# Performance work log

Measured on AMD Instinct MI355X. Metric: run time of the kernel, lower is better.

The kernel has to match this reference:

```python
import jax, jax.numpy as jnp
import numpy as np

N_ENT = 100000


def setup_inputs() -> dict:
    key = jax.random.key(0)
    ks = jax.random.split(key, 10)
    B, D, O, R, E = 50000, 128, 128, 8, 200000
    return {
        "embeddings": jax.random.normal(ks[0], (N_ENT, D), dtype=jnp.float32),
        "head_e": jax.random.normal(ks[1], (B, D), dtype=jnp.float32),
        "tail_e": jax.random.normal(ks[2], (B, D), dtype=jnp.float32),
        "relation_kernel": jax.random.normal(ks[3], (R, D, O), dtype=jnp.float32),
        "self_kernel": jax.random.normal(ks[4], (D, O), dtype=jnp.float32),
        "edge_val": jax.random.uniform(ks[5], (R, E), dtype=jnp.float32),
        "head_idx": jax.random.randint(ks[6], (B,), 0, N_ENT, dtype=jnp.int32),
        "tail_idx": jax.random.randint(ks[7], (B,), 0, N_ENT, dtype=jnp.int32),
        "edge_src": jax.random.randint(ks[8], (R, E), 0, N_ENT, dtype=jnp.int32),
        "edge_dst": jax.random.randint(ks[9], (R, E), 0, N_ENT, dtype=jnp.int32),
    }


def reference(embeddings, head_e, tail_e, relation_kernel, self_kernel,
              edge_val, head_idx, tail_idx, edge_src, edge_dst):
    # Per-relation SpMM: sum_emb[r, row] = sum_{edges e of r with src=row} val[e] * embeddings[dst[e]]
    def spmm(src, dst, val):
        return jax.ops.segment_sum(embeddings[dst] * val[:, None], src,
                                   num_segments=embeddings.shape[0])
    sum_emb = jax.vmap(spmm)(edge_src, edge_dst, edge_val)  # [R, N, D]

    head_update = jnp.take(sum_emb, head_idx, axis=1)  # [R, B, D]
    tail_update = jnp.take(sum_emb, tail_idx, axis=1)  # [R, B, D]

    head_output = head_e @ self_kernel + jnp.einsum('rbd,rdo->bo', head_update, relation_kernel)
    tail_output = tail_e @ self_kernel + jnp.einsum('rbd,rdo->bo', tail_update, relation_kernel)
    return (jax.nn.sigmoid(head_output), jax.nn.sigmoid(tail_output))
```

## Files before the change

### kernel.cpp

```cpp
#include <hip/hip_runtime.h>
#include <hip/hip_bf16.h>
#include <math.h>

#define N_ENT 100000
#define NB    50000
#define NE    200000
#define RR    8
#define NETOT (RR * NE)
#define NSEG  (RR * N_ENT)

typedef float f32x4  __attribute__((ext_vector_type(4)));
typedef short s16x8  __attribute__((ext_vector_type(8)));

__device__ __forceinline__ void split2(float x, short& h, short& l)
{
    unsigned uh = __float_as_uint(x) & 0xffff0000u;
    h = (short)(uh >> 16);
    float r = x - __uint_as_float(uh);
    l = (short)(__float_as_uint(r) >> 16);
}

__global__ __launch_bounds__(256)
void ktconv_k(const float* __restrict__ rel_k, const float* __restrict__ self_k,
              short* __restrict__ Kth, short* __restrict__ Ktl)
{
    const int r = blockIdx.x;
    const float* src = (r < 8) ? rel_k + (size_t)r * 16384 : self_k;
    short* oh = Kth + (size_t)r * 16384;
    short* ol = Ktl + (size_t)r * 16384;
    for (int i = 0; i < 64; ++i) {
        int ix = i * 256 + threadIdx.x;
        int d = ix >> 7, o = ix & 127;
        short h, l;
        split2(src[ix], h, l);
        oh[o * 128 + d] = h;
        ol[o * 128 + d] = l;
    }
}

template<bool FINAL, bool ACCUM>
__global__ __launch_bounds__(256)
void gemm_mfma_k(const float* __restrict__ X, int xstride,
                 const short* __restrict__ Kth, const short* __restrict__ Ktl,
                 int nkc,
                 const float* __restrict__ Abuf, const int* __restrict__ idx,
                 float* __restrict__ out, int nrows)
{
    __shared__ short Bh[128][136];
    __shared__ short Bl[128][136];

    const int t     = threadIdx.x;
    const int wv    = t >> 6;
    const int lane  = t & 63;
    const int col16 = lane & 15;
    const int g     = lane >> 4;
    const int rowbase = blockIdx.x * 128 + wv * 32;

    f32x4 acc[2][8];
#pragma unroll
    for (int m = 0; m < 2; ++m)
#pragma unroll
        for (int c = 0; c < 8; ++c) acc[m][c] = (f32x4){0.f, 0.f, 0.f, 0.f};

    for (int kc = 0; kc < nkc; ++kc) {
        __syncthreads();
        {
            const s16x8* gh = (const s16x8*)(Kth + (size_t)kc * 16384);
            const s16x8* gl = (const s16x8*)(Ktl + (size_t)kc * 16384);
#pragma unroll
            for (int i = 0; i < 8; ++i) {
                int f = t + i * 256;
                int o = f >> 4, c = f & 15;
                *(s16x8*)&Bh[o][c * 8] = gh[f];
                *(s16x8*)&Bl[o][c * 8] = gl[f];
            }
        }
        __syncthreads();

#pragma unroll
        for (int s = 0; s < 4; ++s) {
            s16x8 ah[2], al[2];
#pragma unroll
            for (int m = 0; m < 2; ++m) {
                int r = rowbase + m * 16 + col16;
                if (r > nrows - 1) r = nrows - 1;
                const float* xp = X + (size_t)r * xstride + kc * 128 + s * 32 + g * 8;
                float4 u0 = *(const float4*)xp;
                float4 u1 = *(const float4*)(xp + 4);
                float u[8] = {u0.x, u0.y, u0.z, u0.w, u1.x, u1.y, u1.z, u1.w};
#pragma unroll
                for (int j = 0; j < 8; ++j) {
                    short h, l; split2(u[j], h, l);
                    ah[m][j] = h; al[m][j] = l;
                }
            }
#pragma unroll
            for (int c = 0; c < 8; ++c) {
                s16x8 bh = *(const s16x8*)&Bh[c * 16 + col16][s * 32 + g * 8];
                s16x8 bl = *(const s16x8*)&Bl[c * 16 + col16][s * 32 + g * 8];
#pragma unroll
                for (int m = 0; m < 2; ++m) {
                    acc[m][c] = __builtin_amdgcn_mfma_f32_16x16x32_bf16(ah[m], bh, acc[m][c], 0, 0, 0);
                    acc[m][c] = __builtin_amdgcn_mfma_f32_16x16x32_bf16(ah[m], bl, acc[m][c], 0, 0, 0);
                    acc[m][c] = __builtin_amdgcn_mfma_f32_16x16x32_bf16(al[m], bh, acc[m][c], 0, 0, 0);
                }
            }
        }
    }

#pragma unroll
    for (int m = 0; m < 2; ++m) {
#pragma unroll
        for (int j = 0; j < 4; ++j) {
            int row = rowbase + m * 16 + g * 4 + j;
            if (row >= nrows) continue;
            float* op = out + (size_t)row * 128;
            if (FINAL) {
                int gi = idx[row];
                const float* Ar = Abuf + (size_t)gi * 128;
#pragma unroll
                for (int c = 0; c < 8; ++c) {
                    int col = c * 16 + col16;
                    float x = acc[m][c][j] + Ar[col];
                    op[col] = 1.f / (1.f + __expf(-x));
                }
            } else if (ACCUM) {
#pragma unroll
                for (int c = 0; c < 8; ++c) {
                    int col = c * 16 + col16;
                    op[col] += acc[m][c][j];
                }
            } else {
#pragma unroll
                for (int c = 0; c < 8; ++c)
                    op[c * 16 + col16] = acc[m][c][j];
            }
        }
    }
}

__global__ __launch_bounds__(256)
void count_k(const int* __restrict__ edge_src, unsigned* __restrict__ cnt)
{
    int g = blockIdx.x * 256 + threadIdx.x;
    int r = g / NE;
    int src = edge_src[g];
    atomicAdd(&cnt[r * N_ENT + src], 1u);
}

__global__ __launch_bounds__(256)
void scan1_k(const unsigned* __restrict__ cnt, unsigned* __restrict__ offs,
             unsigned* __restrict__ bsum)
{
    __shared__ unsigned s[256];
    const int t = threadIdx.x;
    const int base = blockIdx.x * 1024;
    unsigned v[4], sum = 0;
#pragma unroll
    for (int i = 0; i < 4; ++i) {
        int ix = base + t * 4 + i;
        v[i] = (ix < NSEG) ? cnt[ix] : 0u;
        sum += v[i];
    }
    s[t] = sum; __syncthreads();
    for (int off = 1; off < 256; off <<= 1) {
        unsigned x = (t >= off) ? s[t - off] : 0u;
        __syncthreads();
        s[t] += x;
        __syncthreads();
    }
    unsigned run = s[t] - sum;
#pragma unroll
    for (int i = 0; i < 4; ++i) {
        int ix = base + t * 4 + i;
        if (ix < NSEG) offs[ix] = run;
        run += v[i];
    }
    if (t == 255) bsum[blockIdx.x] = s[255];
}

__global__ __launch_bounds__(256)
void scan2_k(unsigned* __restrict__ bsum, int nb)
{
    __shared__ unsigned s[256];
    __shared__ unsigned carry;
    const int t = threadIdx.x;
    if (t == 0) carry = 0;
    __syncthreads();
    for (int base = 0; base < nb; base += 256) {
        unsigned v = (base + t < nb) ? bsum[base + t] : 0u;
        s[t] = v; __syncthreads();
        for (int off = 1; off < 256; off <<= 1) {
            unsigned x = (t >= off) ? s[t - off] : 0u;
            __syncthreads();
            s[t] += x;
            __syncthreads();
        }
        unsigned tot = s[255];
        unsigned excl = s[t] - v + carry;
        if (base + t < nb) bsum[base + t] = excl;
        __syncthreads();
        if (t == 0) carry += tot;
        __syncthreads();
    }
}

__global__ __launch_bounds__(256)
void scan3_k(unsigned* __restrict__ offs, const unsigned* __restrict__ bsum)
{
    const int base = blockIdx.x * 1024;
    unsigned add = bsum[blockIdx.x];
#pragma unroll
    for (int i = 0; i < 4; ++i) {
        int ix = base + threadIdx.x * 4 + i;
        if (ix < NSEG) offs[ix] += add;
    }
    if (blockIdx.x == 0 && threadIdx.x == 0) offs[NSEG] = NETOT;
}

__global__ __launch_bounds__(256)
void fill_k(const int* __restrict__ edge_src, const int* __restrict__ edge_dst,
            const float* __restrict__ edge_val,
            const unsigned* __restrict__ offs, unsigned* __restrict__ cursor,
            int2* __restrict__ recs)
{
    int g = blockIdx.x * 256 + threadIdx.x;
    int r = g / NE;
    int src = edge_src[g];
    int seg = r * N_ENT + src;
    unsigned pos = offs[seg] + atomicAdd(&cursor[seg], 1u);
    int2 rec;
    rec.x = edge_dst[g];
    rec.y = __float_as_int(edge_val[g]);
    recs[pos] = rec;
}

template<int NR>
__global__ __launch_bounds__(256)
void segsum_k(const unsigned* __restrict__ offs_r, const int2* __restrict__ recs,
              const float* __restrict__ emb, float* __restrict__ B)
{
    constexpr int T = 4;
    const int s    = (blockIdx.x * 256 + threadIdx.x) >> 6;
    const int lane = threadIdx.x & 63;
    if (s >= N_ENT) return;

    unsigned e0[NR]; int n[NR];
#pragma unroll
    for (int j = 0; j < NR; ++j) {
        unsigned a = offs_r[(size_t)j * N_ENT + s];
        unsigned b = offs_r[(size_t)j * N_ENT + s + 1];
        e0[j] = a; n[j] = (int)(b - a);
    }

    int2 rec[NR][T];
#pragma unroll
    for (int j = 0; j < NR; ++j)
#pragma unroll
        for (int i = 0; i < T; ++i)
            if (i < n[j]) rec[j][i] = recs[e0[j] + i];

    float2 y[NR][T];
#pragma unroll
    for (int j = 0; j < NR; ++j)
#pragma unroll
        for (int i = 0; i < T; ++i)
            if (i < n[j])
                y[j][i] = *(const float2*)(emb + (size_t)rec[j][i].x * 128 + lane * 2);

    float2 acc[NR];
#pragma unroll
    for (int j = 0; j < NR; ++j) acc[j] = (float2){0.f, 0.f};
#pragma unroll
    for (int j = 0; j < NR; ++j)
#pragma unroll
        for (int i = 0; i < T; ++i)
            if (i < n[j]) {
                float v = __int_as_float(rec[j][i].y);
                acc[j].x = fmaf(v, y[j][i].x, acc[j].x);
                acc[j].y = fmaf(v, y[j][i].y, acc[j].y);
            }

#pragma unroll
    for (int j = 0; j < NR; ++j) {
        for (int i = T; i < n[j]; ++i) {
            int2 rc = recs[e0[j] + i];
            float v = __int_as_float(rc.y);
            float2 yy = *(const float2*)(emb + (size_t)rc.x * 128 + lane * 2);
            acc[j].x = fmaf(v, yy.x, acc[j].x);
            acc[j].y = fmaf(v, yy.y, acc[j].y);
        }
    }

#pragma unroll
    for (int j = 0; j < NR; ++j)
        *(float2*)(B + ((size_t)s * NR + j) * 128 + lane * 2) = acc[j];
}

static void launch_segsum(int nr, const unsigned* offs_r, const int2* recs,
                          const float* emb, float* B, hipStream_t stream)
{
    dim3 blk(256);
    const int blocks = (N_ENT * 64) / 256;
    switch (nr) {
    case 1: segsum_k<1><<<blocks, blk, 0, stream>>>(offs_r, recs, emb, B); break;
    case 2: segsum_k<2><<<blocks, blk, 0, stream>>>(offs_r, recs, emb, B); break;
    case 3: segsum_k<3><<<blocks, blk, 0, stream>>>(offs_r, recs, emb, B); break;
    default: segsum_k<4><<<blocks, blk, 0, stream>>>(offs_r, recs, emb, B); break;
    }
}

extern "C" void kernel_launch(void* const* d_in, const int* in_sizes, int n_in,
                              void* d_out, int out_size, void* d_ws, size_t ws_size,
                              hipStream_t stream)
{
    const float* emb      = (const float*)d_in[0];
    const float* head_e   = (const float*)d_in[1];
    const float* tail_e   = (const float*)d_in[2];
    const float* rel_k    = (const float*)d_in[3];
    const float* self_k   = (const float*)d_in[4];
    const float* edge_val = (const float*)d_in[5];
    const int*   head_idx = (const int*)d_in[6];
    const int*   tail_idx = (const int*)d_in[7];
    const int*   edge_src = (const int*)d_in[8];
    const int*   edge_dst = (const int*)d_in[9];
    float* out = (float*)d_out;

    char* p = (char*)d_ws;
    auto take = [&](size_t bytes) -> char* {
        char* q = p; p += (bytes + 255) & ~(size_t)255; return q;
    };
    float*    A    = (float*)take((size_t)N_ENT * 128 * sizeof(float));
    int2*     recs = (int2*)take((size_t)NETOT * sizeof(int2));
    unsigned* cnt  = (unsigned*)take((size_t)NSEG * sizeof(unsigned));
    unsigned* offs = (unsigned*)take(((size_t)NSEG + 1) * sizeof(unsigned));
    unsigned* bsum = (unsigned*)take(1024 * sizeof(unsigned));
    short*    Kth  = (short*)take((size_t)9 * 16384 * sizeof(short));
    short*    Ktl  = (short*)take((size_t)9 * 16384 * sizeof(short));
    float*    Bbuf = (float*)p;

    size_t used    = (size_t)(p - (char*)d_ws);
    size_t avail   = (ws_size > used) ? ws_size - used : 0;
    size_t per_rel = (size_t)N_ENT * 128 * sizeof(float);
    int RPG = (int)(avail / per_rel);
    if (RPG > 4) RPG = 4;
    if (RPG < 1) RPG = 1;

    const int NB1 = (NSEG + 1023) / 1024;
    dim3 blk(256);

    ktconv_k<<<9, blk, 0, stream>>>(rel_k, self_k, Kth, Ktl);
    hipMemsetAsync(cnt, 0, (size_t)NSEG * sizeof(unsigned), stream);
    count_k<<<NETOT / 256, blk, 0, stream>>>(edge_src, cnt);
    scan1_k<<<NB1, blk, 0, stream>>>(cnt, offs, bsum);
    scan2_k<<<1, blk, 0, stream>>>(bsum, NB1);
    scan3_k<<<NB1, blk, 0, stream>>>(offs, bsum);
    hipMemsetAsync(cnt, 0, (size_t)NSEG * sizeof(unsigned), stream);
    fill_k<<<NETOT / 256, blk, 0, stream>>>(edge_src, edge_dst, edge_val,
                                            offs, cnt, recs);

    const int gy = (N_ENT + 127) / 128;
    int first = 1;
    for (int g0 = 0; g0 < RR; ) {
        int nr = (RR - g0 < RPG) ? RR - g0 : RPG;
        launch_segsum(nr, offs + (size_t)g0 * N_ENT, recs, emb, Bbuf, stream);
        if (first)
            gemm_mfma_k<false, false><<<gy, blk, 0, stream>>>(
                Bbuf, nr * 128,
                Kth + (size_t)g0 * 16384, Ktl + (size_t)g0 * 16384, nr,
                nullptr, nullptr, A, N_ENT);
        else
            gemm_mfma_k<false, true><<<gy, blk, 0, stream>>>(
                Bbuf, nr * 128,
                Kth + (size_t)g0 * 16384, Ktl + (size_t)g0 * 16384, nr,
                nullptr, nullptr, A, N_ENT);
        first = 0;
        g0 += nr;
    }

    const int gb = (NB + 127) / 128;
    gemm_mfma_k<true, false><<<gb, blk, 0, stream>>>(
        head_e, 128, Kth + (size_t)8 * 16384, Ktl + (size_t)8 * 16384, 1,
        A, head_idx, out, NB);
    gemm_mfma_k<true, false><<<gb, blk, 0, stream>>>(
        tail_e, 128, Kth + (size_t)8 * 16384, Ktl + (size_t)8 * 16384, 1,
        A, tail_idx, out + (size_t)NB * 128, NB);
}
```

Baseline: 688.9 us.

## Record atomic rank in count pass and stage segsum gathers via LDS

```diff
diff --git a/kernel.cpp b/kernel.cpp
--- a/kernel.cpp
+++ b/kernel.cpp
@@ -18,6 +18,13 @@
     h = (short)(uh >> 16);
     float r = x - __uint_as_float(uh);
     l = (short)(__float_as_uint(r) >> 16);
+}
+
+__device__ __forceinline__ void glds16(const float* g, float* l)
+{
+    __builtin_amdgcn_global_load_lds(
+        (const __attribute__((address_space(1))) void*)g,
+        (__attribute__((address_space(3))) void*)l, 16, 0, 0);
 }
 
 __global__ __launch_bounds__(256)
@@ -140,12 +147,14 @@
 }
 
 __global__ __launch_bounds__(256)
-void count_k(const int* __restrict__ edge_src, unsigned* __restrict__ cnt)
+void count_k(const int* __restrict__ edge_src, unsigned* __restrict__ cnt,
+             unsigned char* __restrict__ rank)
 {
     int g = blockIdx.x * 256 + threadIdx.x;
     int r = g / NE;
     int src = edge_src[g];
-    atomicAdd(&cnt[r * N_ENT + src], 1u);
+    unsigned old = atomicAdd(&cnt[r * N_ENT + src], 1u);
+    rank[g] = (unsigned char)old;
 }
 
 __global__ __launch_bounds__(256)
@@ -221,14 +230,15 @@
 __global__ __launch_bounds__(256)
 void fill_k(const int* __restrict__ edge_src, const int* __restrict__ edge_dst,
             const float* __restrict__ edge_val,
-            const unsigned* __restrict__ offs, unsigned* __restrict__ cursor,
+            const unsigned* __restrict__ offs,
+            const unsigned char* __restrict__ rank,
             int2* __restrict__ recs)
 {
     int g = blockIdx.x * 256 + threadIdx.x;
     int r = g / NE;
     int src = edge_src[g];
     int seg = r * N_ENT + src;
-    unsigned pos = offs[seg] + atomicAdd(&cursor[seg], 1u);
+    unsigned pos = offs[seg] + rank[g];
     int2 rec;
     rec.x = edge_dst[g];
     rec.y = __float_as_int(edge_val[g]);
@@ -241,50 +251,67 @@
               const float* __restrict__ emb, float* __restrict__ B)
 {
     constexpr int T = 4;
+    constexpr int SLOTS = NR * T;
+    __shared__ float stage[4][SLOTS * 128];
+
     const int s    = (blockIdx.x * 256 + threadIdx.x) >> 6;
+    const int wv   = threadIdx.x >> 6;
     const int lane = threadIdx.x & 63;
     if (s >= N_ENT) return;
 
-    unsigned e0[NR]; int n[NR];
+    unsigned a[NR]; int n[NR];
 #pragma unroll
     for (int j = 0; j < NR; ++j) {
-        unsigned a = offs_r[(size_t)j * N_ENT + s];
-        unsigned b = offs_r[(size_t)j * N_ENT + s + 1];
-        e0[j] = a; n[j] = (int)(b - a);
+        unsigned lo = offs_r[(size_t)j * N_ENT + s];
+        unsigned hi = offs_r[(size_t)j * N_ENT + s + 1];
+        a[j] = lo; n[j] = (int)(hi - lo);
     }
 
     int2 rec[NR][T];
 #pragma unroll
+    for (int j = 0; j < NR; ++j) {
+#pragma unroll
+        for (int i = 0; i < T; ++i) {
+            int ii = (i < n[j]) ? i : (n[j] - 1);
+            if (ii < 0) ii = 0;
+            unsigned pos = a[j] + (unsigned)ii;
+            if (pos > (unsigned)(NETOT - 1)) pos = NETOT - 1;
+            rec[j][i] = recs[pos];
+        }
+    }
+
+    float* myst = &stage[wv][0];
+#pragma unroll
+    for (int j = 0; j < NR; ++j) {
+#pragma unroll
+        for (int ip = 0; ip < T / 2; ++ip) {
+            int r0 = rec[j][2 * ip].x;
+            int r1 = rec[j][2 * ip + 1].x;
+            int row = (lane < 32) ? r0 : r1;
+            const float* g = emb + (size_t)row * 128 + (lane & 31) * 4;
+            glds16(g, myst + (j * T + 2 * ip) * 128);
+        }
+    }
+    asm volatile("s_waitcnt vmcnt(0)" ::: "memory");
+    __builtin_amdgcn_sched_barrier(0);
+
+    float2 acc[NR];
+#pragma unroll
+    for (int j = 0; j < NR; ++j) acc[j] = (float2){0.f, 0.f};
+#pragma unroll
     for (int j = 0; j < NR; ++j)
 #pragma unroll
-        for (int i = 0; i < T; ++i)
-            if (i < n[j]) rec[j][i] = recs[e0[j] + i];
-
-    float2 y[NR][T];
-#pragma unroll
-    for (int j = 0; j < NR; ++j)
-#pragma unroll
-        for (int i = 0; i < T; ++i)
-            if (i < n[j])
-                y[j][i] = *(const float2*)(emb + (size_t)rec[j][i].x * 128 + lane * 2);
-
-    float2 acc[NR];
-#pragma unroll
-    for (int j = 0; j < NR; ++j) acc[j] = (float2){0.f, 0.f};
-#pragma unroll
-    for (int j = 0; j < NR; ++j)
-#pragma unroll
-        for (int i = 0; i < T; ++i)
-            if (i < n[j]) {
-                float v = __int_as_float(rec[j][i].y);
-                acc[j].x = fmaf(v, y[j][i].x, acc[j].x);
-                acc[j].y = fmaf(v, y[j][i].y, acc[j].y);
-            }
+        for (int i = 0; i < T; ++i) {
+            float2 y = *(const float2*)&myst[(j * T + i) * 128 + lane * 2];
+            float v = (i < n[j]) ? __int_as_float(rec[j][i].y) : 0.f;
+            acc[j].x = fmaf(v, y.x, acc[j].x);
+            acc[j].y = fmaf(v, y.y, acc[j].y);
+        }
 
 #pragma unroll
     for (int j = 0; j < NR; ++j) {
         for (int i = T; i < n[j]; ++i) {
-            int2 rc = recs[e0[j] + i];
+            int2 rc = recs[a[j] + i];
             float v = __int_as_float(rc.y);
             float2 yy = *(const float2*)(emb + (size_t)rc.x * 128 + lane * 2);
             acc[j].x = fmaf(v, yy.x, acc[j].x);
@@ -330,14 +357,15 @@
     auto take = [&](size_t bytes) -> char* {
         char* q = p; p += (bytes + 255) & ~(size_t)255; return q;
     };
-    float*    A    = (float*)take((size_t)N_ENT * 128 * sizeof(float));
-    int2*     recs = (int2*)take((size_t)NETOT * sizeof(int2));
-    unsigned* cnt  = (unsigned*)take((size_t)NSEG * sizeof(unsigned));
-    unsigned* offs = (unsigned*)take(((size_t)NSEG + 1) * sizeof(unsigned));
-    unsigned* bsum = (unsigned*)take(1024 * sizeof(unsigned));
-    short*    Kth  = (short*)take((size_t)9 * 16384 * sizeof(short));
-    short*    Ktl  = (short*)take((size_t)9 * 16384 * sizeof(short));
-    float*    Bbuf = (float*)p;
+    float*         A    = (float*)take((size_t)N_ENT * 128 * sizeof(float));
+    int2*          recs = (int2*)take((size_t)NETOT * sizeof(int2));
+    unsigned*      cnt  = (unsigned*)take((size_t)NSEG * sizeof(unsigned));
+    unsigned*      offs = (unsigned*)take(((size_t)NSEG + 1) * sizeof(unsigned));
+    unsigned*      bsum = (unsigned*)take(1024 * sizeof(unsigned));
+    unsigned char* rank = (unsigned char*)take((size_t)NETOT);
+    short*         Kth  = (short*)take((size_t)9 * 16384 * sizeof(short));
+    short*         Ktl  = (short*)take((size_t)9 * 16384 * sizeof(short));
+    float*         Bbuf = (float*)p;
 
     size_t used    = (size_t)(p - (char*)d_ws);
     size_t avail   = (ws_size > used) ? ws_size - used : 0;
@@ -351,13 +379,12 @@
 
     ktconv_k<<<9, blk, 0, stream>>>(rel_k, self_k, Kth, Ktl);
     hipMemsetAsync(cnt, 0, (size_t)NSEG * sizeof(unsigned), stream);
-    count_k<<<NETOT / 256, blk, 0, stream>>>(edge_src, cnt);
+    count_k<<<NETOT / 256, blk, 0, stream>>>(edge_src, cnt, rank);
     scan1_k<<<NB1, blk, 0, stream>>>(cnt, offs, bsum);
     scan2_k<<<1, blk, 0, stream>>>(bsum, NB1);
     scan3_k<<<NB1, blk, 0, stream>>>(offs, bsum);
-    hipMemsetAsync(cnt, 0, (size_t)NSEG * sizeof(unsigned), stream);
     fill_k<<<NETOT / 256, blk, 0, stream>>>(edge_src, edge_dst, edge_val,
-                                            offs, cnt, recs);
+                                            offs, rank, recs);
 
     const int gy = (N_ENT + 127) / 128;
     int first = 1;
```

New measurement: 616.3 us. 1.12x faster.
